# Optimization experiments

Measured on AMD Instinct MI355X. Metric: run time of the kernel, lower is better.

The kernel has to match this reference:

```python
import jax, jax.numpy as jnp
import numpy as np

PRIME = 2147483647  # 2^31 - 1, MinHash modulus
GAMMA = 0.3
NUM_HEADS = 8


def minhash_sketch(ids, a, b):
    # ids: (B, L, S) int64 atom ids; a,b: (K,) hash coefficients
    # h[b,l,s,k] = (a[k]*id + b[k]) mod PRIME ; signature = min over the set axis S
    h = (ids[..., None] * a + b) % PRIME          # (B, L, S, K)
    return h.min(axis=2)                          # (B, L, K)


def jaccard_from_signatures(sig_q, sig_k):
    # sig_q: (B, Lq, K), sig_k: (B, Lk, K) -> (B, Lq, Lk) fraction of matching slots.
    # Scan over the K hash slots to avoid materializing a (B,Lq,Lk,K) tensor.
    B, Lq, K = sig_q.shape
    Lk = sig_k.shape[1]

    def step(acc, cols):
        qc, kc = cols                              # (B,Lq), (B,Lk)
        return acc + (qc[:, :, None] == kc[:, None, :]).astype(jnp.float32), None

    init = jnp.zeros((B, Lq, Lk), jnp.float32)
    xs = (jnp.moveaxis(sig_q, -1, 0), jnp.moveaxis(sig_k, -1, 0))
    acc, _ = jax.lax.scan(step, init, xs)
    return acc / K


def symdiff_from_jaccard(jacc, size_q, size_k):
    # |A ∩ B| = J/(1+J) * (|A|+|B|)  =>  |A Δ B| = (|A|+|B|) * (1-J)/(1+J)
    tot = size_q[:, :, None] + size_k[:, None, :]   # (B, Lq, Lk)
    return tot * (1.0 - jacc) / (1.0 + jacc)


def setup_inputs() -> dict:
    key = jax.random.key(0)
    ks = jax.random.split(key, 12)
    B, Lq, Lk, E, S, K, V = 4, 1024, 1024, 512, 8, 128, 32000
    w = lambda k: (jax.random.normal(k, (E, E), jnp.float32) * 0.02)
    return {
        "query": jax.random.normal(ks[0], (B, Lq, E), jnp.float32),
        "key": jax.random.normal(ks[1], (B, Lk, E), jnp.float32),
        "value": jax.random.normal(ks[2], (B, Lk, E), jnp.float32),
        "token_sets_q": jax.random.randint(ks[3], (B, Lq, S), 0, V).astype(jnp.int64),
        "token_sets_k": jax.random.randint(ks[4], (B, Lk, S), 0, V).astype(jnp.int64),
        "hash_a": jax.random.randint(ks[5], (K,), 1, PRIME - 1).astype(jnp.int64),
        "hash_b": jax.random.randint(ks[6], (K,), 0, PRIME - 1).astype(jnp.int64),
        "Wq": w(ks[7]), "bq": jnp.zeros((E,), jnp.float32),
        "Wk": w(ks[8]), "bk": jnp.zeros((E,), jnp.float32),
        "Wv": w(ks[9]), "bv": jnp.zeros((E,), jnp.float32),
        "Wo": w(ks[10]), "bo": jnp.zeros((E,), jnp.float32),
    }


def reference(query, key, value, token_sets_q, token_sets_k, hash_a, hash_b,
              Wq, bq, Wk, bk, Wv, bv, Wo, bo):
    B, Lq, E = query.shape
    Lk = key.shape[1]
    H = NUM_HEADS
    d = E // H

    # in-projections (torch Linear: x @ W^T + b); q,k are computed but the
    # attention scores come solely from the token-set kernel (gating disabled)
    q = query @ Wq.T + bq
    k = key @ Wk.T + bk
    v = (value @ Wv.T + bv).reshape(B, Lk, H, d).transpose(0, 2, 1, 3)  # (B,H,Lk,d)

    # MinHash sketches of per-token atom sets -> estimated Jaccard -> Δ-RBF score
    sig_q = minhash_sketch(token_sets_q, hash_a, hash_b)   # (B,Lq,K)
    sig_k = minhash_sketch(token_sets_k, hash_a, hash_b)   # (B,Lk,K)
    jacc = jaccard_from_signatures(sig_q, sig_k)           # (B,Lq,Lk)

    S = token_sets_q.shape[-1]
    size_q = jnp.full((B, Lq), S, jnp.float32)             # uniform CSR offsets -> |set| = S
    size_k = jnp.full((B, Lk), S, jnp.float32)
    delta = symdiff_from_jaccard(jacc, size_q, size_k)
    scores = jnp.exp(-GAMMA * delta)                       # (B,Lq,Lk), shared by all heads

    attn = jax.nn.softmax(scores, axis=-1)                 # no masks, no causal, dropout=0
    ctx = jnp.einsum('bqk,bhkd->bqhd', attn, v).reshape(B, Lq, E)
    return ctx @ Wo.T + bo
```

## Files before the change

### kernel.cpp

```cpp
#include <hip/hip_runtime.h>
#include <hip/hip_bf16.h>
#include <stdint.h>

#define PRIME 2147483647u
#define GAMMA 0.3f
#define K_HASH 128
#define S_SET 8
#define NB 4
#define LQ 1024
#define LK 1024
#define EDIM 512

typedef __attribute__((ext_vector_type(8))) short short8;
typedef __attribute__((ext_vector_type(4))) float f32x4;

static __device__ __forceinline__ unsigned short f2bf(float f) {
    unsigned u = __builtin_bit_cast(unsigned, f);
    u += 0x7FFFu + ((u >> 16) & 1u);
    return (unsigned short)(u >> 16);
}

__global__ __launch_bounds__(128) void sig_kernel(
        const int* __restrict__ ts_q, const int* __restrict__ ts_k,
        const int* __restrict__ ha, const int* __restrict__ hb,
        int* __restrict__ sig_q, int* __restrict__ sig_k) {
    int blk = blockIdx.x;
    const int* ts = (blk < NB * LQ) ? ts_q : ts_k;
    int*      sig = (blk < NB * LQ) ? sig_q : sig_k;
    int idx = blk & (NB * LQ - 1);
    int k = threadIdx.x;
    unsigned long long a  = (unsigned)ha[k];
    unsigned long long bb = (unsigned)hb[k];
    __shared__ int ids[S_SET];
    if (k < S_SET) ids[k] = ts[idx * S_SET + k];
    __syncthreads();
    unsigned mn = 0xFFFFFFFFu;
    #pragma unroll
    for (int s = 0; s < S_SET; s++) {
        unsigned long long x = a * (unsigned long long)(unsigned)ids[s] + bb;
        x = (x & PRIME) + (x >> 31);
        x = (x & PRIME) + (x >> 31);
        unsigned r = (unsigned)x;
        if (r >= PRIME) r -= PRIME;
        mn = (r < mn) ? r : mn;
    }
    sig[idx * K_HASH + k] = (int)mn;
}

__global__ __launch_bounds__(256) void jaccard_kernel(
        const int* __restrict__ sig_q, const int* __restrict__ sig_k,
        unsigned short* __restrict__ P) {
    __shared__ int Qs[64 * 32];
    __shared__ int Ks[64 * 32];
    __shared__ float lut[K_HASH + 1];
    int tid = threadIdx.x;
    if (tid <= K_HASH) {
        float r = (float)(K_HASH - tid) / (float)(K_HASH + tid);
        float score = expf(-GAMMA * (2.0f * S_SET) * r);
        lut[tid] = expf(score);
    }
    int b  = blockIdx.z;
    int q0 = blockIdx.y * 64, j0 = blockIdx.x * 64;
    const int* sq = sig_q + ((size_t)b * LQ + q0) * K_HASH;
    const int* sk = sig_k + ((size_t)b * LK + j0) * K_HASH;
    int tx = tid & 15, ty = tid >> 4;
    int cnt[4][4] = {};
    int srow = tid >> 2, gbase = (tid & 3) * 2;
    #pragma unroll 1
    for (int ch = 0; ch < 4; ch++) {
        __syncthreads();
        const int4* gq = (const int4*)(sq + srow * K_HASH + ch * 32);
        const int4* gk = (const int4*)(sk + srow * K_HASH + ch * 32);
        #pragma unroll
        for (int u = 0; u < 2; u++) {
            int g = gbase + u;
            int sg = ((g + (srow >> 2)) & 7) * 4;
            *(int4*)&Qs[srow * 32 + sg] = gq[g];
            *(int4*)&Ks[srow * 32 + sg] = gk[g];
        }
        __syncthreads();
        #pragma unroll
        for (int cc = 0; cc < 8; cc++) {
            int4 qv[4], kv[4];
            #pragma unroll
            for (int i = 0; i < 4; i++) {
                int r = ty * 4 + i;
                qv[i] = *(const int4*)&Qs[r * 32 + (((cc + (r >> 2)) & 7) * 4)];
            }
            #pragma unroll
            for (int j = 0; j < 4; j++) {
                int r = tx * 4 + j;
                kv[j] = *(const int4*)&Ks[r * 32 + (((cc + (r >> 2)) & 7) * 4)];
            }
            #pragma unroll
            for (int i = 0; i < 4; i++)
                #pragma unroll
                for (int j = 0; j < 4; j++)
                    cnt[i][j] += (qv[i].x == kv[j].x) + (qv[i].y == kv[j].y)
                               + (qv[i].z == kv[j].z) + (qv[i].w == kv[j].w);
        }
    }
    unsigned short* Pb = P + (size_t)b * LQ * LK;
    #pragma unroll
    for (int i = 0; i < 4; i++) {
        int q = q0 + ty * 4 + i;
        ushort4 o;
        o.x = f2bf(lut[cnt[i][0]]);
        o.y = f2bf(lut[cnt[i][1]]);
        o.z = f2bf(lut[cnt[i][2]]);
        o.w = f2bf(lut[cnt[i][3]]);
        *(ushort4*)&Pb[(size_t)q * LK + j0 + tx * 4] = o;
    }
}

__global__ __launch_bounds__(256) void rowsum_kernel(
        const unsigned short* __restrict__ P, float* __restrict__ invs) {
    int wave = threadIdx.x >> 6, lane = threadIdx.x & 63;
    int row = blockIdx.x * 4 + wave;
    const uint4* p4 = (const uint4*)(P + (size_t)row * LK);
    float s = 0.f;
    for (int t = lane; t < LK / 8; t += 64) {
        uint4 v = p4[t];
        unsigned w[4] = {v.x, v.y, v.z, v.w};
        #pragma unroll
        for (int i = 0; i < 4; i++) {
            s += __builtin_bit_cast(float, w[i] << 16);
            s += __builtin_bit_cast(float, w[i] & 0xFFFF0000u);
        }
    }
    #pragma unroll
    for (int off = 32; off > 0; off >>= 1) s += __shfl_down(s, off, 64);
    if (lane == 0) invs[row] = 1.0f / s;
}

#define EPI_ROWBIAS  0
#define EPI_ROWSCALE 1
#define EPI_COLBIAS  2

template<int AF32, int BF32, int OUTF32, int MODE>
__global__ __launch_bounds__(256) void btgemm_kernel(
        const void* __restrict__ Av, const void* __restrict__ Bv,
        void* __restrict__ Cv,
        const float* __restrict__ biasf,
        const float* __restrict__ scalef,
        int M, int N, int Kd,
        long long strideA, long long strideB, long long strideC,
        long long strideS) {
    __shared__ unsigned short As[64 * 32];
    __shared__ unsigned short Bs[64 * 32];
    int z = blockIdx.z;
    int m0 = blockIdx.y * 64, n0 = blockIdx.x * 64;
    int tid = threadIdx.x;
    int w = tid >> 6, lane = tid & 63;
    int wm = (w & 1) * 32, wn = (w >> 1) * 32;
    f32x4 acc[2][2] = {};
    int srow = tid >> 2, scol = (tid & 3) * 8;
    const float*          Af = (const float*)Av
                               + (size_t)z * strideA + (size_t)(m0 + srow) * Kd + scol;
    const unsigned short* Ah = (const unsigned short*)Av
                               + (size_t)z * strideA + (size_t)(m0 + srow) * Kd + scol;
    const float*          Bf = (const float*)Bv
                               + (size_t)z * strideB + (size_t)(n0 + srow) * Kd + scol;
    const unsigned short* Bh = (const unsigned short*)Bv
                               + (size_t)z * strideB + (size_t)(n0 + srow) * Kd + scol;
    int mrow = lane & 15, kg = lane >> 4;
    for (int k0 = 0; k0 < Kd; k0 += 32) {
        unsigned short* da = &As[srow * 32 + scol];
        if (AF32) {
            float4 v0 = *(const float4*)(Af + k0);
            float4 v1 = *(const float4*)(Af + k0 + 4);
            da[0] = f2bf(v0.x); da[1] = f2bf(v0.y);
            da[2] = f2bf(v0.z); da[3] = f2bf(v0.w);
            da[4] = f2bf(v1.x); da[5] = f2bf(v1.y);
            da[6] = f2bf(v1.z); da[7] = f2bf(v1.w);
        } else {
            *(uint4*)da = *(const uint4*)(Ah + k0);
        }
        unsigned short* db = &Bs[srow * 32 + scol];
        if (BF32) {
            float4 v0 = *(const float4*)(Bf + k0);
            float4 v1 = *(const float4*)(Bf + k0 + 4);
            db[0] = f2bf(v0.x); db[1] = f2bf(v0.y);
            db[2] = f2bf(v0.z); db[3] = f2bf(v0.w);
            db[4] = f2bf(v1.x); db[5] = f2bf(v1.y);
            db[6] = f2bf(v1.z); db[7] = f2bf(v1.w);
        } else {
            *(uint4*)db = *(const uint4*)(Bh + k0);
        }
        __syncthreads();
        short8 af[2], bfr[2];
        #pragma unroll
        for (int s = 0; s < 2; s++) {
            af[s]  = *(const short8*)&As[(wm + s * 16 + mrow) * 32 + kg * 8];
            bfr[s] = *(const short8*)&Bs[(wn + s * 16 + mrow) * 32 + kg * 8];
        }
        #pragma unroll
        for (int i = 0; i < 2; i++)
            #pragma unroll
            for (int j = 0; j < 2; j++)
                acc[i][j] = __builtin_amdgcn_mfma_f32_16x16x32_bf16(
                                af[i], bfr[j], acc[i][j], 0, 0, 0);
        __syncthreads();
    }
    const float* sc = scalef + (size_t)z * strideS;
    int col = lane & 15, rbase = (lane >> 4) * 4;
    #pragma unroll
    for (int i = 0; i < 2; i++) {
        #pragma unroll
        for (int j = 0; j < 2; j++) {
            #pragma unroll
            for (int r = 0; r < 4; r++) {
                int gm = m0 + wm + i * 16 + rbase + r;
                int gn = n0 + wn + j * 16 + col;
                float v = acc[i][j][r];
                if (MODE == EPI_ROWBIAS)       v += biasf[gm];
                else if (MODE == EPI_ROWSCALE) v *= sc[gm];
                else                           v += biasf[gn];
                size_t cix = (size_t)z * strideC + (size_t)gm * N + gn;
                if (OUTF32) ((float*)Cv)[cix] = v;
                else        ((unsigned short*)Cv)[cix] = f2bf(v);
            }
        }
    }
}

extern "C" void kernel_launch(void* const* d_in, const int* in_sizes, int n_in,
                              void* d_out, int out_size, void* d_ws, size_t ws_size,
                              hipStream_t stream) {
    const float* value = (const float*)d_in[2];
    const int* tsq = (const int*)d_in[3];
    const int* tsk = (const int*)d_in[4];
    const int* ha  = (const int*)d_in[5];
    const int* hb  = (const int*)d_in[6];
    const float* Wv = (const float*)d_in[11];
    const float* bv = (const float*)d_in[12];
    const float* Wo = (const float*)d_in[13];
    const float* bo = (const float*)d_in[14];
    float* out = (float*)d_out;

    char* ws = (char*)d_ws;
    int* sigq            = (int*)(ws);
    int* sigk            = (int*)(ws + (2ull << 20));
    unsigned short* P    = (unsigned short*)(ws + (4ull << 20));
    float* invs          = (float*)(ws + (12ull << 20));
    unsigned short* Vt   = (unsigned short*)(ws + (12ull << 20) + (1ull << 16));
    unsigned short* ctx  = (unsigned short*)(ws + (17ull << 20));

    sig_kernel<<<2 * NB * LQ, 128, 0, stream>>>(tsq, tsk, ha, hb, sigq, sigk);

    jaccard_kernel<<<dim3(LK / 64, LQ / 64, NB), 256, 0, stream>>>(sigq, sigk, P);

    rowsum_kernel<<<NB * LQ / 4, 256, 0, stream>>>(P, invs);

    btgemm_kernel<1, 1, 0, EPI_ROWBIAS><<<dim3(LK / 64, EDIM / 64, NB), 256, 0, stream>>>(
        Wv, value, Vt, bv, invs, EDIM, LK, EDIM,
        0LL, (long long)LK * EDIM, (long long)EDIM * LK, 0LL);

    btgemm_kernel<0, 0, 0, EPI_ROWSCALE><<<dim3(EDIM / 64, LQ / 64, NB), 256, 0, stream>>>(
        P, Vt, ctx, bv , invs, LQ, EDIM, LK,
        (long long)LQ * LK, (long long)EDIM * LK, (long long)LQ * EDIM,
        (long long)LQ);

    btgemm_kernel<0, 1, 1, EPI_COLBIAS><<<dim3(EDIM / 64, NB * LQ / 64, 1), 256, 0, stream>>>(
        ctx, Wo, out, bo, invs, NB * LQ, EDIM, EDIM,
        0LL, 0LL, 0LL, 0LL);
}
```

Before: 182.8 us.

## Pre-convert GEMM operands to bf16 and double-buffer tiles via direct global-to-LDS loads

Adds a conversion kernel that turns value, Wv and Wo into bf16 once, so every GEMM takes bf16 inputs and skips the per-tile fp32-to-bf16 conversion. The GEMM kernel is rewritten to use 128x64 tiles, LDS double buffering filled with global_load_lds 16-byte loads, and an XOR swizzle on the LDS layout to reduce bank conflicts. The V projection now runs as one batched 512x4096 GEMM instead of one per batch. The cost is an extra kernel launch and an extra pass over the fp32 value and weights, plus more LDS use per block.

```diff
diff --git a/kernel.cpp b/kernel.cpp
--- a/kernel.cpp
+++ b/kernel.cpp
@@ -11,6 +11,7 @@
 #define LK 1024
 #define EDIM 512
 
+typedef unsigned short ushort_t;
 typedef __attribute__((ext_vector_type(8))) short short8;
 typedef __attribute__((ext_vector_type(4))) float f32x4;
 
@@ -18,6 +19,36 @@
     unsigned u = __builtin_bit_cast(unsigned, f);
     u += 0x7FFFu + ((u >> 16) & 1u);
     return (unsigned short)(u >> 16);
+}
+
+static __device__ __forceinline__ void glds16(const void* g, void* l) {
+    __builtin_amdgcn_global_load_lds(
+        (const __attribute__((address_space(1))) unsigned int*)g,
+        (__attribute__((address_space(3))) unsigned int*)l, 16, 0, 0);
+}
+
+#define SWZ(r) ((((r) >> 2) & 3) ^ ((r) & 3))
+
+#define CVT_N0 (NB * LK * EDIM)
+#define CVT_N1 (EDIM * EDIM)
+#define CVT_N2 (EDIM * EDIM)
+__global__ __launch_bounds__(256) void cvt_kernel(
+        const float* __restrict__ v, const float* __restrict__ wv,
+        const float* __restrict__ wo,
+        ushort_t* __restrict__ vb, ushort_t* __restrict__ wvb,
+        ushort_t* __restrict__ wob) {
+    size_t i = ((size_t)blockIdx.x * 256 + threadIdx.x) * 8;
+    const float* src; ushort_t* dst; size_t off;
+    if (i < CVT_N0)                { src = v;  dst = vb;  off = i; }
+    else if (i < CVT_N0 + CVT_N1)  { src = wv; dst = wvb; off = i - CVT_N0; }
+    else                           { src = wo; dst = wob; off = i - CVT_N0 - CVT_N1; }
+    float4 a = *(const float4*)(src + off);
+    float4 b = *(const float4*)(src + off + 4);
+    ushort4 o0, o1;
+    o0.x = f2bf(a.x); o0.y = f2bf(a.y); o0.z = f2bf(a.z); o0.w = f2bf(a.w);
+    o1.x = f2bf(b.x); o1.y = f2bf(b.y); o1.z = f2bf(b.z); o1.w = f2bf(b.w);
+    *(ushort4*)(dst + off)     = o0;
+    *(ushort4*)(dst + off + 4) = o1;
 }
 
 __global__ __launch_bounds__(128) void sig_kernel(
@@ -121,11 +152,11 @@
     float s = 0.f;
     for (int t = lane; t < LK / 8; t += 64) {
         uint4 v = p4[t];
-        unsigned w[4] = {v.x, v.y, v.z, v.w};
+        unsigned wd[4] = {v.x, v.y, v.z, v.w};
         #pragma unroll
         for (int i = 0; i < 4; i++) {
-            s += __builtin_bit_cast(float, w[i] << 16);
-            s += __builtin_bit_cast(float, w[i] & 0xFFFF0000u);
+            s += __builtin_bit_cast(float, wd[i] << 16);
+            s += __builtin_bit_cast(float, wd[i] & 0xFFFF0000u);
         }
     }
     #pragma unroll
@@ -137,88 +168,83 @@
 #define EPI_ROWSCALE 1
 #define EPI_COLBIAS  2
 
-template<int AF32, int BF32, int OUTF32, int MODE>
+template<int OUTF32, int MODE>
 __global__ __launch_bounds__(256) void btgemm_kernel(
-        const void* __restrict__ Av, const void* __restrict__ Bv,
-        void* __restrict__ Cv,
-        const float* __restrict__ biasf,
-        const float* __restrict__ scalef,
-        int M, int N, int Kd,
-        long long strideA, long long strideB, long long strideC,
-        long long strideS) {
-    __shared__ unsigned short As[64 * 32];
-    __shared__ unsigned short Bs[64 * 32];
+        const ushort_t* __restrict__ A, const ushort_t* __restrict__ B,
+        void* __restrict__ C,
+        const float* __restrict__ bias, const float* __restrict__ scale,
+        int lda, int ldb, int ldc, int Kd,
+        long long sA, long long sB, long long sC, long long sS) {
+    __shared__ ushort_t As[2][128 * 32];
+    __shared__ ushort_t Bs[2][64 * 32];
     int z = blockIdx.z;
-    int m0 = blockIdx.y * 64, n0 = blockIdx.x * 64;
+    int m0 = blockIdx.y * 128, n0 = blockIdx.x * 64;
     int tid = threadIdx.x;
     int w = tid >> 6, lane = tid & 63;
-    int wm = (w & 1) * 32, wn = (w >> 1) * 32;
-    f32x4 acc[2][2] = {};
-    int srow = tid >> 2, scol = (tid & 3) * 8;
-    const float*          Af = (const float*)Av
-                               + (size_t)z * strideA + (size_t)(m0 + srow) * Kd + scol;
-    const unsigned short* Ah = (const unsigned short*)Av
-                               + (size_t)z * strideA + (size_t)(m0 + srow) * Kd + scol;
-    const float*          Bf = (const float*)Bv
-                               + (size_t)z * strideB + (size_t)(n0 + srow) * Kd + scol;
-    const unsigned short* Bh = (const unsigned short*)Bv
-                               + (size_t)z * strideB + (size_t)(n0 + srow) * Kd + scol;
+    int wm = (w & 1) * 64, wn = (w >> 1) * 32;
     int mrow = lane & 15, kg = lane >> 4;
-    for (int k0 = 0; k0 < Kd; k0 += 32) {
-        unsigned short* da = &As[srow * 32 + scol];
-        if (AF32) {
-            float4 v0 = *(const float4*)(Af + k0);
-            float4 v1 = *(const float4*)(Af + k0 + 4);
-            da[0] = f2bf(v0.x); da[1] = f2bf(v0.y);
-            da[2] = f2bf(v0.z); da[3] = f2bf(v0.w);
-            da[4] = f2bf(v1.x); da[5] = f2bf(v1.y);
-            da[6] = f2bf(v1.z); da[7] = f2bf(v1.w);
-        } else {
-            *(uint4*)da = *(const uint4*)(Ah + k0);
-        }
-        unsigned short* db = &Bs[srow * 32 + scol];
-        if (BF32) {
-            float4 v0 = *(const float4*)(Bf + k0);
-            float4 v1 = *(const float4*)(Bf + k0 + 4);
-            db[0] = f2bf(v0.x); db[1] = f2bf(v0.y);
-            db[2] = f2bf(v0.z); db[3] = f2bf(v0.w);
-            db[4] = f2bf(v1.x); db[5] = f2bf(v1.y);
-            db[6] = f2bf(v1.z); db[7] = f2bf(v1.w);
-        } else {
-            *(uint4*)db = *(const uint4*)(Bh + k0);
-        }
+
+    int r = tid >> 2, c = (tid & 3) ^ SWZ(r);
+    const ushort_t* pa0 = A + (size_t)z * sA + (size_t)(m0 + r) * lda + c * 8;
+    const ushort_t* pa1 = pa0 + (size_t)64 * lda;
+    const ushort_t* pb  = B + (size_t)z * sB + (size_t)(n0 + r) * ldb + c * 8;
+
+    int aoff[4], boff[2];
+    #pragma unroll
+    for (int i = 0; i < 4; i++) {
+        int R = wm + i * 16 + mrow;
+        aoff[i] = R * 32 + (kg ^ SWZ(R)) * 8;
+    }
+    #pragma unroll
+    for (int j = 0; j < 2; j++) {
+        int R = wn + j * 16 + mrow;
+        boff[j] = R * 32 + (kg ^ SWZ(R)) * 8;
+    }
+
+    f32x4 acc[4][2] = {};
+    int nK = Kd >> 5;
+    glds16(pa0, &As[0][tid * 8]);
+    glds16(pa1, &As[0][2048 + tid * 8]);
+    glds16(pb,  &Bs[0][tid * 8]);
+    for (int i = 0; i < nK; i++) {
         __syncthreads();
-        short8 af[2], bfr[2];
-        #pragma unroll
-        for (int s = 0; s < 2; s++) {
-            af[s]  = *(const short8*)&As[(wm + s * 16 + mrow) * 32 + kg * 8];
-            bfr[s] = *(const short8*)&Bs[(wn + s * 16 + mrow) * 32 + kg * 8];
-        }
-        #pragma unroll
-        for (int i = 0; i < 2; i++)
-            #pragma unroll
-            for (int j = 0; j < 2; j++)
-                acc[i][j] = __builtin_amdgcn_mfma_f32_16x16x32_bf16(
-                                af[i], bfr[j], acc[i][j], 0, 0, 0);
-        __syncthreads();
-    }
-    const float* sc = scalef + (size_t)z * strideS;
+        int cur = i & 1, nxt = cur ^ 1;
+        if (i + 1 < nK) {
+            int k0 = (i + 1) << 5;
+            glds16(pa0 + k0, &As[nxt][tid * 8]);
+            glds16(pa1 + k0, &As[nxt][2048 + tid * 8]);
+            glds16(pb  + k0, &Bs[nxt][tid * 8]);
+        }
+        short8 af[4], bh[2];
+        #pragma unroll
+        for (int ii = 0; ii < 4; ii++) af[ii] = *(const short8*)&As[cur][aoff[ii]];
+        #pragma unroll
+        for (int jj = 0; jj < 2; jj++) bh[jj] = *(const short8*)&Bs[cur][boff[jj]];
+        #pragma unroll
+        for (int ii = 0; ii < 4; ii++)
+            #pragma unroll
+            for (int jj = 0; jj < 2; jj++)
+                acc[ii][jj] = __builtin_amdgcn_mfma_f32_16x16x32_bf16(
+                                  af[ii], bh[jj], acc[ii][jj], 0, 0, 0);
+    }
+
+    const float* sc = scale + (size_t)z * sS;
     int col = lane & 15, rbase = (lane >> 4) * 4;
     #pragma unroll
-    for (int i = 0; i < 2; i++) {
-        #pragma unroll
-        for (int j = 0; j < 2; j++) {
-            #pragma unroll
-            for (int r = 0; r < 4; r++) {
-                int gm = m0 + wm + i * 16 + rbase + r;
-                int gn = n0 + wn + j * 16 + col;
-                float v = acc[i][j][r];
-                if (MODE == EPI_ROWBIAS)       v += biasf[gm];
+    for (int ii = 0; ii < 4; ii++) {
+        #pragma unroll
+        for (int jj = 0; jj < 2; jj++) {
+            #pragma unroll
+            for (int rr = 0; rr < 4; rr++) {
+                int gm = m0 + wm + ii * 16 + rbase + rr;
+                int gn = n0 + wn + jj * 16 + col;
+                float v = acc[ii][jj][rr];
+                if (MODE == EPI_ROWBIAS)       v += bias[gm];
                 else if (MODE == EPI_ROWSCALE) v *= sc[gm];
-                else                           v += biasf[gn];
-                size_t cix = (size_t)z * strideC + (size_t)gm * N + gn;
-                if (OUTF32) ((float*)Cv)[cix] = v;
-                else        ((unsigned short*)Cv)[cix] = f2bf(v);
+                else                           v += bias[gn];
+                size_t cix = (size_t)z * sC + (size_t)gm * ldc + gn;
+                if (OUTF32) ((float*)C)[cix] = v;
+                else        ((ushort_t*)C)[cix] = f2bf(v);
             }
         }
     }
@@ -239,12 +265,18 @@
     float* out = (float*)d_out;
 
     char* ws = (char*)d_ws;
-    int* sigq            = (int*)(ws);
-    int* sigk            = (int*)(ws + (2ull << 20));
-    unsigned short* P    = (unsigned short*)(ws + (4ull << 20));
-    float* invs          = (float*)(ws + (12ull << 20));
-    unsigned short* Vt   = (unsigned short*)(ws + (12ull << 20) + (1ull << 16));
-    unsigned short* ctx  = (unsigned short*)(ws + (17ull << 20));
+    int* sigq        = (int*)(ws);
+    int* sigk        = (int*)(ws + (2ull << 20));
+    ushort_t* P      = (ushort_t*)(ws + (4ull << 20));
+    float* invs      = (float*)(ws + (12ull << 20));
+    ushort_t* Vt     = (ushort_t*)(ws + (12ull << 20) + (1ull << 16));
+    ushort_t* ctx    = (ushort_t*)(ws + (17ull << 20));
+    ushort_t* Vb     = (ushort_t*)(ws + (21ull << 20));
+    ushort_t* Wvb    = (ushort_t*)(ws + (25ull << 20));
+    ushort_t* Wob    = (ushort_t*)(ws + (25ull << 20) + (512ull << 10));
+
+    cvt_kernel<<<(CVT_N0 + CVT_N1 + CVT_N2) / (256 * 8), 256, 0, stream>>>(
+        value, Wv, Wo, Vb, Wvb, Wob);
 
     sig_kernel<<<2 * NB * LQ, 128, 0, stream>>>(tsq, tsk, ha, hb, sigq, sigk);
 
@@ -252,16 +284,16 @@
 
     rowsum_kernel<<<NB * LQ / 4, 256, 0, stream>>>(P, invs);
 
-    btgemm_kernel<1, 1, 0, EPI_ROWBIAS><<<dim3(LK / 64, EDIM / 64, NB), 256, 0, stream>>>(
-        Wv, value, Vt, bv, invs, EDIM, LK, EDIM,
-        0LL, (long long)LK * EDIM, (long long)EDIM * LK, 0LL);
-
-    btgemm_kernel<0, 0, 0, EPI_ROWSCALE><<<dim3(EDIM / 64, LQ / 64, NB), 256, 0, stream>>>(
-        P, Vt, ctx, bv , invs, LQ, EDIM, LK,
-        (long long)LQ * LK, (long long)EDIM * LK, (long long)LQ * EDIM,
-        (long long)LQ);
-
-    btgemm_kernel<0, 1, 1, EPI_COLBIAS><<<dim3(EDIM / 64, NB * LQ / 64, 1), 256, 0, stream>>>(
-        ctx, Wo, out, bo, invs, NB * LQ, EDIM, EDIM,
-        0LL, 0LL, 0LL, 0LL);
-}
+    btgemm_kernel<0, EPI_ROWBIAS><<<dim3(4096 / 64, 512 / 128, 1), 256, 0, stream>>>(
+        Wvb, Vb, Vt, bv, invs ,
+        EDIM, EDIM, NB * LK, EDIM, 0LL, 0LL, 0LL, 0LL);
+
+    btgemm_kernel<0, EPI_ROWSCALE><<<dim3(EDIM / 64, LQ / 128, NB), 256, 0, stream>>>(
+        P, Vt, ctx, bv , invs,
+        LK, NB * LK, EDIM, LK,
+        (long long)LQ * LK, (long long)LK, (long long)LQ * EDIM, (long long)LQ);
+
+    btgemm_kernel<1, EPI_COLBIAS><<<dim3(EDIM / 64, NB * LQ / 128, 1), 256, 0, stream>>>(
+        ctx, Wob, out, bo, invs ,
+        EDIM, EDIM, EDIM, EDIM, 0LL, 0LL, 0LL, 0LL);
+}
```

Measured after the change: 179.7 us. No clear change (-1.7%).
